# Kernel optimization log

Hardware: AMD Instinct MI355X
Metric: run time of the kernel (lower is better)

The kernel has to match this reference:

```python
import jax, jax.numpy as jnp
import numpy as np

DIM = 1024
HEADS = 16
HDIM = DIM // HEADS
MLP_HID = 4096
LN_EPS = 1e-5
NORM_EPS = 1e-12  # F.normalize eps


def _layernorm(x, g, b):
    mu = jnp.mean(x, axis=-1, keepdims=True)
    var = jnp.mean(jnp.square(x - mu), axis=-1, keepdims=True)
    return (x - mu) / jnp.sqrt(var + LN_EPS) * g + b


def _l2norm(x):
    n = jnp.linalg.norm(x, axis=-1, keepdims=True)
    return x / jnp.maximum(n, NORM_EPS)


def setup_inputs() -> dict:
    key = jax.random.key(0)
    ks = jax.random.split(key, 8)
    s = 0.02
    x = jax.random.normal(ks[0], (2, 2048, DIM), dtype=jnp.float32)
    w_qkv = jax.random.normal(ks[1], (3 * DIM, DIM), dtype=jnp.float32) * s  # torch Linear weight (out,in)
    w_proj = jax.random.normal(ks[2], (DIM, DIM), dtype=jnp.float32) * s
    temp = jnp.ones((HEADS, 1, 1), dtype=jnp.float32)
    w1 = jax.random.normal(ks[3], (MLP_HID, DIM), dtype=jnp.float32) * s
    b1 = jnp.zeros((MLP_HID,), dtype=jnp.float32)
    w2 = jax.random.normal(ks[4], (DIM, MLP_HID), dtype=jnp.float32) * s
    b2 = jnp.zeros((DIM,), dtype=jnp.float32)
    ln1_g = jnp.ones((DIM,), dtype=jnp.float32)
    ln1_b = jnp.zeros((DIM,), dtype=jnp.float32)
    ln2_g = jnp.ones((DIM,), dtype=jnp.float32)
    ln2_b = jnp.zeros((DIM,), dtype=jnp.float32)
    return {"x": x, "ln1_g": ln1_g, "ln1_b": ln1_b, "w_qkv": w_qkv,
            "w_proj": w_proj, "temp": temp, "ln2_g": ln2_g, "ln2_b": ln2_b,
            "w1": w1, "b1": b1, "w2": w2, "b2": b2}


def reference(x, ln1_g, ln1_b, w_qkv, w_proj, temp, ln2_g, ln2_b, w1, b1, w2, b2):
    b, n, c = x.shape
    # --- MHSA with L2-normalized q,k and learnable per-head temperature ---
    h = _layernorm(x, ln1_g, ln1_b)
    qkv = h @ w_qkv.T                             # [b,n,3c]
    qkv = qkv.reshape(b, n, 3, HEADS, HDIM).transpose(2, 0, 3, 1, 4)  # [3,b,h,n,d]
    q, k, v = qkv[0], qkv[1], qkv[2]
    q = _l2norm(q)
    k = _l2norm(k)
    attn = jnp.einsum('bhnd,bhmd->bhnm', q, k) * temp  # temp [h,1,1] broadcasts
    attn = jax.nn.softmax(attn, axis=-1)
    out = jnp.einsum('bhnm,bhmd->bhnd', attn, v)       # [b,h,n,d]
    out = out.transpose(0, 2, 1, 3).reshape(b, n, c)
    x = x + out @ w_proj.T
    # --- MLP ---
    h = _layernorm(x, ln2_g, ln2_b)
    h = jax.nn.gelu(h @ w1.T + b1, approximate=False)
    x = x + h @ w2.T + b2
    return x
```

## Files before the change

### kernel.cpp

```cpp
#include <hip/hip_runtime.h>
#include <cstdint>
#include <cstddef>

typedef unsigned short u16;
typedef __attribute__((ext_vector_type(8))) short short8;
typedef __attribute__((ext_vector_type(4))) float f32x4;
typedef __attribute__((ext_vector_type(4))) float float4v;
typedef __attribute__((ext_vector_type(4))) u16 u16x4;

__device__ __forceinline__ u16 f2bf(float f) {
  union { float f; uint32_t u; } v; v.f = f;
  uint32_t u = v.u;
  return (u16)((u + 0x7FFFu + ((u >> 16) & 1u)) >> 16);
}
__device__ __forceinline__ float bf2f(u16 s) {
  union { uint32_t u; float f; } v; v.u = ((uint32_t)s) << 16; return v.f;
}

__device__ __forceinline__ float fast_exp2(float x) {
#if __has_builtin(__builtin_amdgcn_exp2f)
  return __builtin_amdgcn_exp2f(x);
#else
  return exp2f(x);
#endif
}

__device__ __forceinline__ void gload16(const u16* g, u16* l) {
  __builtin_amdgcn_global_load_lds((const __attribute__((address_space(1))) void*)g,
                                   (__attribute__((address_space(3))) void*)l,
                                   16, 0, 0);
}

#define SBAR __builtin_amdgcn_sched_barrier(0)

__global__ __launch_bounds__(256) void k_cvt4(const float* __restrict__ wqkv, const float* __restrict__ wproj,
                                              const float* __restrict__ w1, const float* __restrict__ w2,
                                              u16* __restrict__ o_qkv, u16* __restrict__ o_proj,
                                              u16* __restrict__ o_w1, u16* __restrict__ o_w2) {
  const int total = 3145728;
  int stride = gridDim.x * 256;
  for (int i = blockIdx.x * 256 + threadIdx.x; i < total; i += stride) {
    const float* src; u16* dst; int loc;
    if (i < 786432)       { src = wqkv;  dst = o_qkv;  loc = i; }
    else if (i < 1048576) { src = wproj; dst = o_proj; loc = i - 786432; }
    else if (i < 2097152) { src = w1;    dst = o_w1;   loc = i - 1048576; }
    else                  { src = w2;    dst = o_w2;   loc = i - 2097152; }
    float4v v = *(const float4v*)(src + (size_t)loc * 4);
    u16x4 o;
    #pragma unroll
    for (int j = 0; j < 4; j++) o[j] = f2bf(v[j]);
    *(u16x4*)(dst + (size_t)loc * 4) = o;
  }
}

__global__ __launch_bounds__(256) void k_ln(const float* __restrict__ x, const float* __restrict__ g,
                                            const float* __restrict__ b, u16* __restrict__ out) {
  int row = blockIdx.x, tid = threadIdx.x;
  int wid = tid >> 6;
  const float* xr = x + (size_t)row * 1024;
  float4v v = *(const float4v*)(xr + tid * 4);
  float s = v[0] + v[1] + v[2] + v[3];
  float sq = v[0]*v[0] + v[1]*v[1] + v[2]*v[2] + v[3]*v[3];
  #pragma unroll
  for (int m = 1; m <= 32; m <<= 1) { s += __shfl_xor(s, m); sq += __shfl_xor(sq, m); }
  __shared__ float ss[4], ssq[4];
  if ((tid & 63) == 0) { ss[wid] = s; ssq[wid] = sq; }
  __syncthreads();
  s = ss[0] + ss[1] + ss[2] + ss[3];
  sq = ssq[0] + ssq[1] + ssq[2] + ssq[3];
  float mu = s * (1.0f/1024.0f);
  float var = sq * (1.0f/1024.0f) - mu*mu;
  float rs = rsqrtf(var + 1e-5f);
  u16x4 o;
  #pragma unroll
  for (int j = 0; j < 4; j++) {
    float y = (v[j] - mu) * rs * g[tid*4+j] + b[tid*4+j];
    o[j] = f2bf(y);
  }
  *(u16x4*)(out + (size_t)row * 1024 + tid * 4) = o;
}

__global__ __launch_bounds__(256) void k_redln(const float* __restrict__ x, const u16* __restrict__ P,
                                               const float* __restrict__ g, const float* __restrict__ b,
                                               float* __restrict__ x1, u16* __restrict__ h2) {
  int row = blockIdx.x, tid = threadIdx.x;
  int wid = tid >> 6;
  size_t off = (size_t)row * 1024 + tid * 4;
  float4v v = *(const float4v*)(x + off);
  #pragma unroll
  for (int z = 0; z < 4; z++) {
    u16x4 p = *(const u16x4*)(P + (size_t)z * 4194304 + off);
    #pragma unroll
    for (int j = 0; j < 4; j++) v[j] += bf2f(p[j]);
  }
  *(float4v*)(x1 + off) = v;
  float s = v[0] + v[1] + v[2] + v[3];
  float sq = v[0]*v[0] + v[1]*v[1] + v[2]*v[2] + v[3]*v[3];
  #pragma unroll
  for (int m = 1; m <= 32; m <<= 1) { s += __shfl_xor(s, m); sq += __shfl_xor(sq, m); }
  __shared__ float ss[4], ssq[4];
  if ((tid & 63) == 0) { ss[wid] = s; ssq[wid] = sq; }
  __syncthreads();
  s = ss[0] + ss[1] + ss[2] + ss[3];
  sq = ssq[0] + ssq[1] + ssq[2] + ssq[3];
  float mu = s * (1.0f/1024.0f);
  float var = sq * (1.0f/1024.0f) - mu*mu;
  float rs = rsqrtf(var + 1e-5f);
  u16x4 o;
  #pragma unroll
  for (int j = 0; j < 4; j++) o[j] = f2bf((v[j] - mu) * rs * g[tid*4+j] + b[tid*4+j]);
  *(u16x4*)(h2 + off) = o;
}

template<int EPI>
__global__ __launch_bounds__(512, 2) void k_g256(const u16* __restrict__ A, const u16* __restrict__ B,
                                                 const float* __restrict__ bias, u16* __restrict__ Cb,
                                                 int M, int N, int K, int Ksub) {
  extern __shared__ __align__(16) u16 smem[];
  int tid = threadIdx.x;
  int gx = gridDim.x;
  int lin = blockIdx.y * gx + blockIdx.x;
  int nwg = gx * gridDim.y;
  int cpx = nwg >> 3;
  int swz = (lin & 7) * cpx + (lin >> 3);
  int bx = swz % gx, by = swz / gx;
  int m0 = by * 256, n0 = bx * 256;
  int kbase = blockIdx.z * Ksub;
  int wid = tid >> 6, lane = tid & 63;
  int wm = wid >> 2, wn = wid & 3;
  int l15 = lane & 15, l16 = lane >> 4;

  f32x4 acc[8][4] = {};
  int nt = Ksub >> 6;

  auto STAGE = [&](int bsel, int kb) {
    #pragma unroll
    for (int st = 0; st < 2; st++) {
      u16* abase = smem + bsel*32768 + st*16384;
      u16* bbase = abase + 8192;
      int kbs = kb + st*32;
      #pragma unroll
      for (int i = 0; i < 2; i++) {
        int c = i*512 + tid;
        int R = c >> 3, p = c & 7;
        int sp = p ^ (R & 7);
        int r = 2*R + (sp >> 2);
        int g = sp & 3;
        gload16(A + (size_t)(m0 + r)*K + kbs + g*8, abase + c*8);
        gload16(B + (size_t)(n0 + r)*K + kbs + g*8, bbase + c*8);
      }
    }
  };

  STAGE(0, kbase);

  for (int t = 0; t < nt; ++t) {
    int sl = t & 1;
    asm volatile("s_waitcnt vmcnt(0)" ::: "memory");
    SBAR;
    __builtin_amdgcn_s_barrier();
    SBAR;
    if (t + 1 < nt) STAGE(sl ^ 1, kbase + (t + 1) * 64);
    #pragma unroll
    for (int st = 0; st < 2; st++) {
      const u16* ab = smem + sl*32768 + st*16384;
      const u16* bb = ab + 8192;
      short8 af[8], bf[4];
      #pragma unroll
      for (int mf = 0; mf < 8; mf++) {
        int r = wm*128 + mf*16 + l15;
        int R = r >> 1;
        int sp = ((r & 1)*4 + l16) ^ (R & 7);
        af[mf] = *(const short8*)(ab + R*64 + sp*8);
      }
      #pragma unroll
      for (int nf = 0; nf < 4; nf++) {
        int r = wn*64 + nf*16 + l15;
        int R = r >> 1;
        int sp = ((r & 1)*4 + l16) ^ (R & 7);
        bf[nf] = *(const short8*)(bb + R*64 + sp*8);
      }
      asm volatile("s_waitcnt lgkmcnt(0)" ::: "memory");
      SBAR;
      __builtin_amdgcn_s_setprio(1);
      #pragma unroll
      for (int mf = 0; mf < 8; mf++)
        #pragma unroll
        for (int nf = 0; nf < 4; nf++)
          acc[mf][nf] = __builtin_amdgcn_mfma_f32_16x16x32_bf16(af[mf], bf[nf], acc[mf][nf], 0, 0, 0);
      __builtin_amdgcn_s_setprio(0);
    }
  }

  size_t zoff = (EPI == 6) ? (size_t)blockIdx.z * M * N : 0;
  #pragma unroll
  for (int mf = 0; mf < 8; mf++) {
    #pragma unroll
    for (int nf = 0; nf < 4; nf++) {
      int col = n0 + wn*64 + nf*16 + l15;
      #pragma unroll
      for (int r = 0; r < 4; r++) {
        int row = m0 + wm*128 + mf*16 + l16*4 + r;
        float v = acc[mf][nf][r];
        if constexpr (EPI == 2) { v += bias[col]; v = 0.5f*v*(1.0f + erff(v*0.70710678118f)); }
        Cb[zoff + (size_t)row*N + col] = f2bf(v);
      }
    }
  }
}

template<int NP, int HASB>
__global__ __launch_bounds__(256) void k_red(const float* __restrict__ base, const float* __restrict__ bias,
                                             const u16* __restrict__ P, size_t zstride, float* __restrict__ out) {
  int i = blockIdx.x * 256 + threadIdx.x;
  float4v v = *(const float4v*)(base + (size_t)i * 4);
  if constexpr (HASB) {
    float4v bb = *(const float4v*)(bias + (size_t)(i & 255) * 4);
    #pragma unroll
    for (int j = 0; j < 4; j++) v[j] += bb[j];
  }
  #pragma unroll
  for (int z = 0; z < NP; z++) {
    u16x4 p = *(const u16x4*)(P + (size_t)z * zstride + (size_t)i * 4);
    #pragma unroll
    for (int j = 0; j < 4; j++) v[j] += bf2f(p[j]);
  }
  *(float4v*)(out + (size_t)i * 4) = v;
}

__global__ __launch_bounds__(256) void k_prep(const u16* __restrict__ qkv, const float* __restrict__ temp,
                                              u16* __restrict__ Qn, u16* __restrict__ Kn, u16* __restrict__ Vt) {
  int grp = blockIdx.x, bh = blockIdx.y;
  int b = bh >> 4, h = bh & 15;
  int tid = threadIdx.x;
  int n0 = grp * 64;
  __shared__ __align__(16) u16 vs[64*64];
  float tmp = temp[h] * 1.44269504f;
  int j8 = tid & 7;
  #pragma unroll
  for (int pass = 0; pass < 2; pass++) {
    int tl = pass*32 + (tid >> 3);
    size_t roff = (size_t)((b*2048) + n0 + tl) * 3072 + h*64 + j8*8;
    short8 q8 = *(const short8*)(qkv + roff);
    short8 k8 = *(const short8*)(qkv + roff + 1024);
    short8 v8 = *(const short8*)(qkv + roff + 2048);
    float qv[8], kv[8];
    float sq = 0.f, sk = 0.f;
    #pragma unroll
    for (int jj = 0; jj < 8; jj++) {
      qv[jj] = bf2f((u16)q8[jj]); sq += qv[jj]*qv[jj];
      kv[jj] = bf2f((u16)k8[jj]); sk += kv[jj]*kv[jj];
    }
    sq += __shfl_xor(sq, 1); sq += __shfl_xor(sq, 2); sq += __shfl_xor(sq, 4);
    sk += __shfl_xor(sk, 1); sk += __shfl_xor(sk, 2); sk += __shfl_xor(sk, 4);
    float qs = tmp / fmaxf(sqrtf(sq), 1e-12f);
    float ksc = 1.0f / fmaxf(sqrtf(sk), 1e-12f);
    short8 qo, ko;
    #pragma unroll
    for (int jj = 0; jj < 8; jj++) {
      qo[jj] = (short)f2bf(qv[jj] * qs);
      ko[jj] = (short)f2bf(kv[jj] * ksc);
    }
    size_t obase = ((size_t)bh*2048 + n0 + tl)*64 + j8*8;
    *(short8*)(Qn + obase) = qo;
    *(short8*)(Kn + obase) = ko;
    *(short8*)&vs[tl*64 + j8*8] = v8;
  }
  __syncthreads();
  int d = tid & 63, chunk = tid >> 6;
  u16 vals[16];
  #pragma unroll
  for (int jj = 0; jj < 16; jj++) vals[jj] = vs[(chunk*16 + jj)*64 + d];
  short8 w0, w1v;
  #pragma unroll
  for (int j = 0; j < 8; j++) { w0[j] = (short)vals[j]; w1v[j] = (short)vals[8+j]; }
  size_t vo = ((size_t)bh*64 + d)*2048 + n0 + chunk*16;
  *(short8*)(Vt + vo) = w0;
  *(short8*)(Vt + vo + 8) = w1v;
}

__device__ __forceinline__ int akey(int row) { return (row & 3) | (((row >> 3) & 1) << 2); }

__global__ __launch_bounds__(256) void k_attn(const u16* __restrict__ Qn, const u16* __restrict__ Kn,
                                              const u16* __restrict__ Vt, const float* __restrict__ temp,
                                              u16* __restrict__ Out) {
  __shared__ __align__(16) u16 Ks[2][64*64];
  __shared__ __align__(16) u16 Vs[2][64*64];
  int lin = blockIdx.y * gridDim.x + blockIdx.x;
  int c = lin & 7, t5 = lin >> 3;
  int bh = c*4 + (t5 >> 4);
  int qg = t5 & 15;
  int b = bh >> 4, h = bh & 15;
  int tid = threadIdx.x, wid = tid >> 6, lane = tid & 63;
  int l15 = lane & 15, l16 = lane >> 4;
  size_t base = (size_t)bh * 2048 * 64;
  size_t vbase = (size_t)bh * 64 * 2048;
  int q0 = qg*128 + wid*32;
  float m2 = fabsf(temp[h]) * 1.44269504f;
  short8 qf[2][2];
  #pragma unroll
  for (int g = 0; g < 2; g++)
    #pragma unroll
    for (int ks = 0; ks < 2; ks++)
      qf[g][ks] = *(const short8*)(Qn + base + (size_t)(q0 + g*16 + l15)*64 + ks*32 + l16*8);
  f32x4 o[2][4] = {};
  float lrow[2] = {0.f, 0.f};
  int prow = (l15 & 3) + 8*(l15 >> 2);

  auto STAGE = [&](int bsel, int kv0) {
    #pragma unroll
    for (int i = 0; i < 2; i++) {
      int cc = i*256 + tid;
      int row = cc >> 3, p = cc & 7;
      int g = p ^ akey(row);
      gload16(Kn + base + (size_t)(kv0 + row)*64 + g*8, &Ks[bsel][(i*256 + wid*64)*8]);
      gload16(Vt + vbase + (size_t)row*2048 + kv0 + g*8, &Vs[bsel][(i*256 + wid*64)*8]);
    }
  };

  STAGE(0, 0);
  __syncthreads();
  int cur = 0;
  for (int kv0 = 0; kv0 < 2048; kv0 += 64) {
    if (kv0 + 64 < 2048) STAGE(cur ^ 1, kv0 + 64);
    f32x4 s[2][4];
    #pragma unroll
    for (int g = 0; g < 2; g++)
      #pragma unroll
      for (int ss = 0; ss < 4; ss++)
        s[g][ss] = f32x4{-m2, -m2, -m2, -m2};
    __builtin_amdgcn_s_setprio(1);
    #pragma unroll
    for (int dks = 0; dks < 2; dks++) {
      #pragma unroll
      for (int ss = 0; ss < 4; ss++) {
        int row = (ss & 1)*4 + (ss >> 1)*32 + prow;
        short8 kf = *(const short8*)&Ks[cur][row*64 + ((dks*4 + l16) ^ akey(row))*8];
        s[0][ss] = __builtin_amdgcn_mfma_f32_16x16x32_bf16(kf, qf[0][dks], s[0][ss], 0, 0, 0);
        s[1][ss] = __builtin_amdgcn_mfma_f32_16x16x32_bf16(kf, qf[1][dks], s[1][ss], 0, 0, 0);
      }
    }
    __builtin_amdgcn_s_setprio(0);
    short8 pf[2][2];
    #pragma unroll
    for (int g = 0; g < 2; g++) {
      float tsum = 0.f;
      #pragma unroll
      for (int kvs = 0; kvs < 2; kvs++) {
        float e[8];
        #pragma unroll
        for (int r = 0; r < 4; r++) {
          e[r]   = fast_exp2(s[g][kvs*2][r]);
          e[4+r] = fast_exp2(s[g][kvs*2+1][r]);
        }
        #pragma unroll
        for (int r = 0; r < 8; r++) tsum += e[r];
        union { uint32_t u[4]; short8 v; } pu;
        #pragma unroll
        for (int w = 0; w < 4; w++) {
          uint32_t pk;
          asm("v_cvt_pk_bf16_f32 %0, %1, %2" : "=v"(pk) : "v"(e[2*w]), "v"(e[2*w+1]));
          pu.u[w] = pk;
        }
        pf[g][kvs] = pu.v;
      }
      lrow[g] += tsum;
    }
    __builtin_amdgcn_s_setprio(1);
    #pragma unroll
    for (int kvs = 0; kvs < 2; kvs++) {
      short8 vf[4];
      #pragma unroll
      for (int dt = 0; dt < 4; dt++) {
        int row = dt*16 + l15;
        vf[dt] = *(const short8*)&Vs[cur][row*64 + (((kvs*4 + l16) ^ akey(row))*8)];
      }
      #pragma unroll
      for (int dt = 0; dt < 4; dt++) {
        o[0][dt] = __builtin_amdgcn_mfma_f32_16x16x32_bf16(vf[dt], pf[0][kvs], o[0][dt], 0, 0, 0);
        o[1][dt] = __builtin_amdgcn_mfma_f32_16x16x32_bf16(vf[dt], pf[1][kvs], o[1][dt], 0, 0, 0);
      }
    }
    __builtin_amdgcn_s_setprio(0);
    __syncthreads();
    cur ^= 1;
  }
  #pragma unroll
  for (int g = 0; g < 2; g++) {
    float l = lrow[g];
    l += __shfl_xor(l, 16);
    l += __shfl_xor(l, 32);
    float rl = 1.0f / l;
    int tok = b*2048 + q0 + g*16 + l15;
    #pragma unroll
    for (int dt = 0; dt < 4; dt++) {
      u16x4 ov;
      #pragma unroll
      for (int r = 0; r < 4; r++) ov[r] = f2bf(o[g][dt][r] * rl);
      *(u16x4*)(Out + (size_t)tok*1024 + h*64 + dt*16 + l16*4) = ov;
    }
  }
}

static constexpr size_t OFF_WQKV  = 0;
static constexpr size_t OFF_WPROJ = OFF_WQKV  + 6291456;
static constexpr size_t OFF_W1    = OFF_WPROJ + 2097152;
static constexpr size_t OFF_W2    = OFF_W1    + 8388608;
static constexpr size_t OFF_HBF   = OFF_W2    + 8388608;
static constexpr size_t OFF_QKVBF = OFF_HBF   + 8388608;
static constexpr size_t OFF_QN    = OFF_QKVBF + 25165824;
static constexpr size_t OFF_KN    = OFF_QN    + 8388608;
static constexpr size_t OFF_VT    = OFF_KN    + 8388608;
static constexpr size_t OFF_AOUT  = OFF_VT    + 8388608;
static constexpr size_t OFF_H2BF  = OFF_AOUT  + 8388608;
static constexpr size_t OFF_X1    = OFF_H2BF  + 8388608;
static constexpr size_t OFF_HID   = OFF_X1    + 16777216;

extern "C" void kernel_launch(void* const* d_in, const int* in_sizes, int n_in,
                              void* d_out, int out_size, void* d_ws, size_t ws_size,
                              hipStream_t stream) {
  (void)in_sizes; (void)n_in; (void)out_size; (void)ws_size;
  const float* x     = (const float*)d_in[0];
  const float* ln1g  = (const float*)d_in[1];
  const float* ln1b  = (const float*)d_in[2];
  const float* wqkv  = (const float*)d_in[3];
  const float* wproj = (const float*)d_in[4];
  const float* temp  = (const float*)d_in[5];
  const float* ln2g  = (const float*)d_in[6];
  const float* ln2b  = (const float*)d_in[7];
  const float* w1    = (const float*)d_in[8];
  const float* b1    = (const float*)d_in[9];
  const float* w2    = (const float*)d_in[10];
  const float* b2    = (const float*)d_in[11];

  char* ws = (char*)d_ws;
  u16* wqkv_bf  = (u16*)(ws + OFF_WQKV);
  u16* wproj_bf = (u16*)(ws + OFF_WPROJ);
  u16* w1_bf    = (u16*)(ws + OFF_W1);
  u16* w2_bf    = (u16*)(ws + OFF_W2);
  u16* h_bf     = (u16*)(ws + OFF_HBF);
  u16* h2_bf    = (u16*)(ws + OFF_H2BF);
  u16* qkv_bf   = (u16*)(ws + OFF_QKVBF);
  u16* Qn       = (u16*)(ws + OFF_QN);
  u16* Kn       = (u16*)(ws + OFF_KN);
  u16* Vt       = (u16*)(ws + OFF_VT);
  u16* aout_bf  = (u16*)(ws + OFF_AOUT);
  float* x1     = (float*)(ws + OFF_X1);
  u16* hid_bf   = (u16*)(ws + OFF_HID);
  u16* part_p   = (u16*)(ws + OFF_HID);
  u16* part_m   = (u16*)(ws + OFF_QN);
  float* outf   = (float*)d_out;

  static bool attr_done = false;
  if (!attr_done) {
    hipFuncSetAttribute((const void*)k_g256<2>, hipFuncAttributeMaxDynamicSharedMemorySize, 131072);
    hipFuncSetAttribute((const void*)k_g256<4>, hipFuncAttributeMaxDynamicSharedMemorySize, 131072);
    hipFuncSetAttribute((const void*)k_g256<6>, hipFuncAttributeMaxDynamicSharedMemorySize, 131072);
    attr_done = true;
  }

  k_cvt4<<<2048, 256, 0, stream>>>(wqkv, wproj, w1, w2, wqkv_bf, wproj_bf, w1_bf, w2_bf);

  k_ln<<<4096, 256, 0, stream>>>(x, ln1g, ln1b, h_bf);
  k_g256<4><<<dim3(12, 16), 512, 131072, stream>>>(h_bf, wqkv_bf, nullptr, qkv_bf, 4096, 3072, 1024, 1024);
  k_prep<<<dim3(32, 32), 256, 0, stream>>>(qkv_bf, temp, Qn, Kn, Vt);
  k_attn<<<dim3(16, 32), 256, 0, stream>>>(Qn, Kn, Vt, temp, aout_bf);
  k_g256<6><<<dim3(4, 16, 4), 512, 131072, stream>>>(aout_bf, wproj_bf, nullptr, part_p, 4096, 1024, 1024, 256);
  k_redln<<<4096, 256, 0, stream>>>(x, part_p, ln2g, ln2b, x1, h2_bf);
  k_g256<2><<<dim3(16, 16), 512, 131072, stream>>>(h2_bf, w1_bf, b1, hid_bf, 4096, 4096, 1024, 1024);
  k_g256<6><<<dim3(4, 16, 4), 512, 131072, stream>>>(hid_bf, w2_bf, nullptr, part_m, 4096, 1024, 4096, 1024);
  k_red<4,1><<<4096, 256, 0, stream>>>(x1, b2, part_m, 4194304, outf);
}
```

Baseline: 235.5 us.

## Split attention KV range across two blocks and fuse weight conversion with LN1

The attention kernel now splits the 2048-key range into two halves along grid z. Each half writes unnormalized fp32 partial outputs and row sums, and a new combine kernel adds them and normalizes. This doubles the attention block count (512 to 1024) to fill more compute units, at the cost of extra fp32 partial writes and reads plus one more launch. Separately, the weight-conversion and first layernorm kernels merge into one launch so their work can run concurrently. The split relies on a fixed max (temperature bound), so the partials can be summed without rescaling.

```diff
diff --git a/kernel.cpp b/kernel.cpp
--- a/kernel.cpp
+++ b/kernel.cpp
@@ -33,29 +33,31 @@
 
 #define SBAR __builtin_amdgcn_sched_barrier(0)
 
-__global__ __launch_bounds__(256) void k_cvt4(const float* __restrict__ wqkv, const float* __restrict__ wproj,
-                                              const float* __restrict__ w1, const float* __restrict__ w2,
-                                              u16* __restrict__ o_qkv, u16* __restrict__ o_proj,
-                                              u16* __restrict__ o_w1, u16* __restrict__ o_w2) {
-  const int total = 3145728;
-  int stride = gridDim.x * 256;
-  for (int i = blockIdx.x * 256 + threadIdx.x; i < total; i += stride) {
-    const float* src; u16* dst; int loc;
-    if (i < 786432)       { src = wqkv;  dst = o_qkv;  loc = i; }
-    else if (i < 1048576) { src = wproj; dst = o_proj; loc = i - 786432; }
-    else if (i < 2097152) { src = w1;    dst = o_w1;   loc = i - 1048576; }
-    else                  { src = w2;    dst = o_w2;   loc = i - 2097152; }
-    float4v v = *(const float4v*)(src + (size_t)loc * 4);
-    u16x4 o;
-    #pragma unroll
-    for (int j = 0; j < 4; j++) o[j] = f2bf(v[j]);
-    *(u16x4*)(dst + (size_t)loc * 4) = o;
-  }
-}
-
-__global__ __launch_bounds__(256) void k_ln(const float* __restrict__ x, const float* __restrict__ g,
-                                            const float* __restrict__ b, u16* __restrict__ out) {
-  int row = blockIdx.x, tid = threadIdx.x;
+__global__ __launch_bounds__(256) void k_cvtln(const float* __restrict__ wqkv, const float* __restrict__ wproj,
+                                               const float* __restrict__ w1, const float* __restrict__ w2,
+                                               u16* __restrict__ o_qkv, u16* __restrict__ o_proj,
+                                               u16* __restrict__ o_w1, u16* __restrict__ o_w2,
+                                               const float* __restrict__ x, const float* __restrict__ g,
+                                               const float* __restrict__ bb, u16* __restrict__ ln_out) {
+  int blk = blockIdx.x, tid = threadIdx.x;
+  if (blk < 2048) {
+    const int total = 3145728;
+    const int stride = 2048 * 256;
+    for (int i = blk * 256 + tid; i < total; i += stride) {
+      const float* src; u16* dst; int loc;
+      if (i < 786432)       { src = wqkv;  dst = o_qkv;  loc = i; }
+      else if (i < 1048576) { src = wproj; dst = o_proj; loc = i - 786432; }
+      else if (i < 2097152) { src = w1;    dst = o_w1;   loc = i - 1048576; }
+      else                  { src = w2;    dst = o_w2;   loc = i - 2097152; }
+      float4v v = *(const float4v*)(src + (size_t)loc * 4);
+      u16x4 o;
+      #pragma unroll
+      for (int j = 0; j < 4; j++) o[j] = f2bf(v[j]);
+      *(u16x4*)(dst + (size_t)loc * 4) = o;
+    }
+    return;
+  }
+  int row = blk - 2048;
   int wid = tid >> 6;
   const float* xr = x + (size_t)row * 1024;
   float4v v = *(const float4v*)(xr + tid * 4);
@@ -73,11 +75,8 @@
   float rs = rsqrtf(var + 1e-5f);
   u16x4 o;
   #pragma unroll
-  for (int j = 0; j < 4; j++) {
-    float y = (v[j] - mu) * rs * g[tid*4+j] + b[tid*4+j];
-    o[j] = f2bf(y);
-  }
-  *(u16x4*)(out + (size_t)row * 1024 + tid * 4) = o;
+  for (int j = 0; j < 4; j++) o[j] = f2bf((v[j] - mu) * rs * g[tid*4+j] + bb[tid*4+j]);
+  *(u16x4*)(ln_out + (size_t)row * 1024 + tid * 4) = o;
 }
 
 __global__ __launch_bounds__(256) void k_redln(const float* __restrict__ x, const u16* __restrict__ P,
@@ -283,10 +282,11 @@
 
 __global__ __launch_bounds__(256) void k_attn(const u16* __restrict__ Qn, const u16* __restrict__ Kn,
                                               const u16* __restrict__ Vt, const float* __restrict__ temp,
-                                              u16* __restrict__ Out) {
+                                              float* __restrict__ Of, float* __restrict__ Lf) {
   __shared__ __align__(16) u16 Ks[2][64*64];
   __shared__ __align__(16) u16 Vs[2][64*64];
   int lin = blockIdx.y * gridDim.x + blockIdx.x;
+  int z = blockIdx.z;
   int c = lin & 7, t5 = lin >> 3;
   int bh = c*4 + (t5 >> 4);
   int qg = t5 & 15;
@@ -296,6 +296,7 @@
   size_t base = (size_t)bh * 2048 * 64;
   size_t vbase = (size_t)bh * 64 * 2048;
   int q0 = qg*128 + wid*32;
+  int kvlo = z * 1024, kvhi = kvlo + 1024;
   float m2 = fabsf(temp[h]) * 1.44269504f;
   short8 qf[2][2];
   #pragma unroll
@@ -318,11 +319,11 @@
     }
   };
 
-  STAGE(0, 0);
+  STAGE(0, kvlo);
   __syncthreads();
   int cur = 0;
-  for (int kv0 = 0; kv0 < 2048; kv0 += 64) {
-    if (kv0 + 64 < 2048) STAGE(cur ^ 1, kv0 + 64);
+  for (int kv0 = kvlo; kv0 < kvhi; kv0 += 64) {
+    if (kv0 + 64 < kvhi) STAGE(cur ^ 1, kv0 + 64);
     f32x4 s[2][4];
     #pragma unroll
     for (int g = 0; g < 2; g++)
@@ -385,21 +386,40 @@
     __syncthreads();
     cur ^= 1;
   }
+  size_t zo = (size_t)z * 4194304;
   #pragma unroll
   for (int g = 0; g < 2; g++) {
     float l = lrow[g];
     l += __shfl_xor(l, 16);
     l += __shfl_xor(l, 32);
-    float rl = 1.0f / l;
-    int tok = b*2048 + q0 + g*16 + l15;
+    int qi = q0 + g*16 + l15;
+    int row = b*2048 + qi;
+    if (l16 == 0) Lf[(size_t)z*65536 + bh*2048 + qi] = l;
     #pragma unroll
     for (int dt = 0; dt < 4; dt++) {
-      u16x4 ov;
-      #pragma unroll
-      for (int r = 0; r < 4; r++) ov[r] = f2bf(o[g][dt][r] * rl);
-      *(u16x4*)(Out + (size_t)tok*1024 + h*64 + dt*16 + l16*4) = ov;
-    }
-  }
+      float4v ov;
+      #pragma unroll
+      for (int r = 0; r < 4; r++) ov[r] = o[g][dt][r];
+      *(float4v*)(Of + zo + (size_t)row*1024 + h*64 + dt*16 + l16*4) = ov;
+    }
+  }
+}
+
+__global__ __launch_bounds__(256) void k_acomb(const float* __restrict__ Of, const float* __restrict__ Lf,
+                                               u16* __restrict__ aout) {
+  int row = blockIdx.x, tid = threadIdx.x;
+  int b = row >> 11, qi = row & 2047;
+  int h = tid >> 4;
+  size_t off = (size_t)row * 1024 + tid * 4;
+  float4v o0 = *(const float4v*)(Of + off);
+  float4v o1 = *(const float4v*)(Of + 4194304 + off);
+  float l0 = Lf[(b*16 + h)*2048 + qi];
+  float l1 = Lf[65536 + (b*16 + h)*2048 + qi];
+  float rl = 1.0f / (l0 + l1);
+  u16x4 o;
+  #pragma unroll
+  for (int j = 0; j < 4; j++) o[j] = f2bf((o0[j] + o1[j]) * rl);
+  *(u16x4*)(aout + off) = o;
 }
 
 static constexpr size_t OFF_WQKV  = 0;
@@ -415,6 +435,7 @@
 static constexpr size_t OFF_H2BF  = OFF_AOUT  + 8388608;
 static constexpr size_t OFF_X1    = OFF_H2BF  + 8388608;
 static constexpr size_t OFF_HID   = OFF_X1    + 16777216;
+static constexpr size_t OFF_L     = OFF_HID + 20971520;
 
 extern "C" void kernel_launch(void* const* d_in, const int* in_sizes, int n_in,
                               void* d_out, int out_size, void* d_ws, size_t ws_size,
@@ -449,6 +470,8 @@
   u16* hid_bf   = (u16*)(ws + OFF_HID);
   u16* part_p   = (u16*)(ws + OFF_HID);
   u16* part_m   = (u16*)(ws + OFF_QN);
+  float* Of     = (float*)(ws + OFF_X1);
+  float* Lf     = (float*)(ws + OFF_L);
   float* outf   = (float*)d_out;
 
   static bool attr_done = false;
@@ -459,12 +482,12 @@
     attr_done = true;
   }
 
-  k_cvt4<<<2048, 256, 0, stream>>>(wqkv, wproj, w1, w2, wqkv_bf, wproj_bf, w1_bf, w2_bf);
-
-  k_ln<<<4096, 256, 0, stream>>>(x, ln1g, ln1b, h_bf);
+  k_cvtln<<<6144, 256, 0, stream>>>(wqkv, wproj, w1, w2, wqkv_bf, wproj_bf, w1_bf, w2_bf,
+                                    x, ln1g, ln1b, h_bf);
   k_g256<4><<<dim3(12, 16), 512, 131072, stream>>>(h_bf, wqkv_bf, nullptr, qkv_bf, 4096, 3072, 1024, 1024);
   k_prep<<<dim3(32, 32), 256, 0, stream>>>(qkv_bf, temp, Qn, Kn, Vt);
-  k_attn<<<dim3(16, 32), 256, 0, stream>>>(Qn, Kn, Vt, temp, aout_bf);
+  k_attn<<<dim3(16, 32, 2), 256, 0, stream>>>(Qn, Kn, Vt, temp, Of, Lf);
+  k_acomb<<<4096, 256, 0, stream>>>(Of, Lf, aout_bf);
   k_g256<6><<<dim3(4, 16, 4), 512, 131072, stream>>>(aout_bf, wproj_bf, nullptr, part_p, 4096, 1024, 1024, 256);
   k_redln<<<4096, 256, 0, stream>>>(x, part_p, ln2g, ln2b, x1, h2_bf);
   k_g256<2><<<dim3(16, 16), 512, 131072, stream>>>(h2_bf, w1_bf, b1, hid_bf, 4096, 4096, 1024, 1024);
```

New measurement: 245.4 us. 4.2% more time.
